# Kernel optimization log

Hardware: AMD Instinct MI355X
Metric: run time of the kernel (lower is better)

Reference implementation:

```python
import jax, jax.numpy as jnp
import numpy as np

B, H, W, DIM, WS, SHIFT, NH = 8, 64, 64, 512, 8, 4, 16
NC, NE, HID, GH = 3, 4, 2048, 256
N = WS * WS
nW = (H // WS) * (W // WS)
HD = DIM // NH
LN_EPS = 1e-5


def _static_buffers():
    # SwinV2 log-spaced continuous relative coords table
    r = np.arange(-(WS - 1), WS, dtype=np.float32)
    table = np.stack(np.meshgrid(r, r, indexing='ij'), axis=-1)[None]  # (1,2WS-1,2WS-1,2)
    table = table / (WS - 1) * 8.0
    table = np.sign(table) * np.log2(np.abs(table) + 1.0) / np.log2(8.0)
    # relative position index (N,N)
    coords = np.stack(np.meshgrid(np.arange(WS), np.arange(WS), indexing='ij'))
    cf = coords.reshape(2, -1)
    rel = (cf[:, :, None] - cf[:, None, :]).transpose(1, 2, 0).astype(np.int64)
    rel[..., 0] += WS - 1
    rel[..., 1] += WS - 1
    rel[..., 0] *= 2 * WS - 1
    rpi = rel.sum(-1)
    # shifted-window attention mask (nW,N,N)
    img = np.zeros((1, H, W, 1), np.float32)
    cnt = 0
    sls = (slice(0, -WS), slice(-WS, -SHIFT), slice(-SHIFT, None))
    for hs in sls:
        for ws_ in sls:
            img[:, hs, ws_, :] = cnt
            cnt += 1
    mw = img.reshape(1, H // WS, WS, W // WS, WS, 1).transpose(0, 1, 3, 2, 4, 5).reshape(-1, N)
    am = mw[:, None, :] - mw[:, :, None]
    am = np.where(am != 0, -100.0, 0.0).astype(np.float32)
    return jnp.asarray(table), rpi, jnp.asarray(am)

TABLE, RPI, ATTN_MASK = _static_buffers()


def _ln(x, w, b):
    m = x.mean(-1, keepdims=True)
    v = ((x - m) ** 2).mean(-1, keepdims=True)
    return (x - m) / jnp.sqrt(v + LN_EPS) * w + b


def setup_inputs():
    key = jax.random.key(0)
    ks = iter(jax.random.split(key, 40))
    p = lambda shape: jax.random.normal(next(ks), shape, jnp.float32) * 0.02
    return {
        'x': jax.random.normal(next(ks), (B, H * W, DIM), jnp.float32),
        'qkv_w': p((3 * DIM, DIM)), 'q_bias': p((DIM,)), 'v_bias': p((DIM,)),
        'logit_scale': jnp.log(10.0 * jnp.ones((NH, 1, 1), jnp.float32)),
        'cpb_w1': p((512, 2)), 'cpb_b1': p((512,)), 'cpb_w2': p((NH, 512)),
        'proj_w': p((DIM, DIM)), 'proj_b': jnp.zeros((DIM,), jnp.float32),
        'norm1_w': jnp.ones((DIM,), jnp.float32), 'norm1_b': jnp.zeros((DIM,), jnp.float32),
        'norm2_w': jnp.ones((DIM,), jnp.float32), 'norm2_b': jnp.zeros((DIM,), jnp.float32),
        'exp_w1': p((NE, HID, DIM)), 'exp_b1': jnp.zeros((NE, HID), jnp.float32),
        'exp_w2': p((NE, DIM, HID)), 'exp_b2': jnp.zeros((NE, DIM), jnp.float32),
        'gate_l1_w': p((GH, DIM)), 'gate_l1_b': jnp.zeros((GH,), jnp.float32),
        'gate_fa_w': p((GH, GH)), 'gate_fa_b': jnp.zeros((GH,), jnp.float32),
        'gate_l2_w': p((NE, GH)), 'gate_l2_b': jnp.zeros((NE,), jnp.float32),
        'task_w': p((DIM, DIM)), 'task_b': jnp.zeros((DIM,), jnp.float32),
    }


def reference(x, qkv_w, q_bias, v_bias, logit_scale, cpb_w1, cpb_b1, cpb_w2,
              proj_w, proj_b, norm1_w, norm1_b, norm2_w, norm2_b,
              exp_w1, exp_b1, exp_w2, exp_b2,
              gate_l1_w, gate_l1_b, gate_fa_w, gate_fa_b, gate_l2_w, gate_l2_b,
              task_w, task_b):
    shortcut = x
    # cyclic shift + window partition
    xi = jnp.roll(x.reshape(B, H, W, DIM), (-SHIFT, -SHIFT), axis=(1, 2))
    xw = xi.reshape(B, H // WS, WS, W // WS, WS, DIM).transpose(0, 1, 3, 2, 4, 5).reshape(-1, N, DIM)
    # qkv with q/v bias only (k bias zero)
    qkv_b = jnp.concatenate([q_bias, jnp.zeros_like(v_bias), v_bias])
    qkv = (xw @ qkv_w.T + qkv_b).reshape(-1, N, 3, NH, HD).transpose(2, 0, 3, 1, 4)
    q, k, v = qkv[0], qkv[1], qkv[2]
    # SwinV2 cosine attention
    qn = q / jnp.maximum(jnp.linalg.norm(q, axis=-1, keepdims=True), 1e-12)
    kn = k / jnp.maximum(jnp.linalg.norm(k, axis=-1, keepdims=True), 1e-12)
    scale = jnp.exp(jnp.minimum(logit_scale, jnp.log(100.0)))
    attn = jnp.einsum('bhnd,bhmd->bhnm', qn, kn) * scale
    # continuous relative position bias
    bias_tbl = (jax.nn.relu(TABLE @ cpb_w1.T + cpb_b1) @ cpb_w2.T).reshape(-1, NH)
    rpb = bias_tbl[RPI.reshape(-1)].reshape(N, N, NH).transpose(2, 0, 1)
    attn = attn + (16.0 * jax.nn.sigmoid(rpb))[None]
    # shifted window mask
    attn = attn.reshape(B, nW, NH, N, N) + ATTN_MASK[None, :, None]
    attn = jax.nn.softmax(attn.reshape(-1, NH, N, N), axis=-1)
    out = jnp.einsum('bhnm,bhmd->bnhd', attn, v).reshape(-1, N, DIM)
    out = out @ proj_w.T + proj_b
    # window reverse + reverse shift
    xr = out.reshape(B, H // WS, W // WS, WS, WS, DIM).transpose(0, 1, 3, 2, 4, 5).reshape(B, H, W, DIM)
    xr = jnp.roll(xr, (SHIFT, SHIFT), axis=(1, 2)).reshape(B, H * W, DIM)
    x1 = shortcut + _ln(xr, norm1_w, norm1_b)  # SwinV2 post-norm residual
    # MMoE FFN (inference gating path; dropouts are eval no-ops)
    eo = []
    for e in range(NE):
        h = jax.nn.gelu(x1 @ exp_w1[e].T + exp_b1[e], approximate=False)
        eo.append(h @ exp_w2[e].T + exp_b2[e])
    eo = jnp.stack(eo, axis=-1)  # (B, L, DIM, NE)
    t = x1 @ task_w.T + task_b
    g = jax.nn.relu(t @ gate_l1_w.T + gate_l1_b)
    aw = jax.nn.softmax(g @ gate_fa_w.T + gate_fa_b, axis=-1)
    gate_logits = (g * aw) @ gate_l2_w.T + gate_l2_b
    wts = jax.nn.softmax(gate_logits, axis=-1)  # temperature = 1.0
    moe = jnp.einsum('blde,ble->bld', eo, wts)
    return x1 + _ln(moe, norm2_w, norm2_b)
```

## Files before the change

### kernel.cpp

```cpp
#include <hip/hip_runtime.h>
#include <math.h>

typedef __bf16 bf16;
typedef bf16 bf16x8 __attribute__((ext_vector_type(8)));
typedef bf16 bf16x4_t __attribute__((ext_vector_type(4)));
typedef float f32x4 __attribute__((ext_vector_type(4)));


#define EPI_QKV  0
#define EPI_PROJ 1
#define EPI_BF16 2
#define EPI_RELU 3
#define EPI_F32  4
#define EPI_GELU 5
#define EPI_MOE  6

#define NIN 26

#define GLDS16(gp, lp)                                                    \
    __builtin_amdgcn_global_load_lds(                                     \
        (const __attribute__((address_space(1))) void*)(gp),              \
        (__attribute__((address_space(3))) void*)(lp), 16, 0, 0)

__global__ __launch_bounds__(256) void probe_k(const unsigned short* __restrict__ x,
                                               int* __restrict__ flag)
{
    __shared__ int cnt[256];
    int t = threadIdx.x;
    int bad = 0;
    for (int j = t; j < 4096; j += 256) {
        int e = (x[j] >> 7) & 0xFF;
        if (e >= 132) bad++;
    }
    cnt[t] = bad;
    __syncthreads();
    for (int s = 128; s > 0; s >>= 1) {
        if (t < s) cnt[t] += cnt[t + s];
        __syncthreads();
    }
    if (t == 0) *flag = (cnt[0] > 64) ? 1 : 0;
}

struct ConvArgs {
    const void* src[NIN];
    bf16* dst[NIN];
    int n[NIN];
};

__global__ __launch_bounds__(256) void conv_k(ConvArgs a, const int* __restrict__ flag)
{
    int i = blockIdx.y;
    int n4 = a.n[i] >> 2;
    bf16x4_t* dst = (bf16x4_t*)a.dst[i];
    int stride = gridDim.x * 256;
    if (*flag) {
        const float4* s = (const float4*)a.src[i];
        for (int j = blockIdx.x * 256 + threadIdx.x; j < n4; j += stride) {
            float4 v = s[j];
            dst[j] = (bf16x4_t){(bf16)v.x, (bf16)v.y, (bf16)v.z, (bf16)v.w};
        }
    } else {
        const bf16x4_t* s = (const bf16x4_t*)a.src[i];
        for (int j = blockIdx.x * 256 + threadIdx.x; j < n4; j += stride)
            dst[j] = s[j];
    }
}

__device__ __forceinline__ int win_remap(int r) {
    int win = r >> 6, tok = r & 63;
    int b = win >> 6, wi = win & 63;
    int h = (((wi >> 3) << 3) + (tok >> 3) + 4) & 63;
    int w = (((wi & 7) << 3) + (tok & 7) + 4) & 63;
    return (b << 12) | (h << 6) | w;
}

template<int REMAP_A, int EPI>
__global__ __launch_bounds__(256, 4) void gemm_k(
    const bf16* __restrict__ A, const bf16* __restrict__ Bw,
    void* __restrict__ Cout,
    const bf16* __restrict__ bias, const bf16* __restrict__ bias2,
    const float* __restrict__ wts, int N, int K, int eIdx, int nbm)
{
    __shared__ __attribute__((aligned(16))) bf16 As[128 * 64];
    __shared__ __attribute__((aligned(16))) bf16 Bs[128 * 64];
    const int tid = threadIdx.x;

    const int lin = blockIdx.x;
    const int nbn = N >> 7;
    const int xcd = lin & 7, s = lin >> 3;
    const int nbmx = nbm >> 3;
    const int G = nbmx < 16 ? nbmx : 16;
    const int gsz = G * nbn;
    const int gi = s / gsz, rem = s - gi * gsz;
    const int bn = rem / G, bmi = rem - bn * G;
    const int bm = xcd + 8 * (gi * G + bmi);

    const int wave = tid >> 6, lane = tid & 63;
    const int wm = (wave >> 1) << 6, wn = (wave & 1) << 6;
    const int lrow = lane & 15, quad = lane >> 4;

    const int sr = tid >> 3, sc = tid & 7;
    const int scg = sc ^ (sr & 7);
    int ga[4];
#pragma unroll
    for (int i = 0; i < 4; i++) {
        int r = bm * 128 + sr + i * 32;
        ga[i] = REMAP_A ? win_remap(r) : r;
    }
    const int brow = bn * 128 + sr;
    bf16* lA = As + tid * 8;
    bf16* lB = Bs + tid * 8;

    f32x4 acc[4][4];
#pragma unroll
    for (int i = 0; i < 4; i++)
#pragma unroll
        for (int j = 0; j < 4; j++) acc[i][j] = (f32x4){0.f, 0.f, 0.f, 0.f};

    for (int k0 = 0; k0 < K; k0 += 64) {
        __syncthreads();
#pragma unroll
        for (int i = 0; i < 4; i++) {
            GLDS16(A + (size_t)ga[i] * K + k0 + scg * 8, lA + i * 2048);
            GLDS16(Bw + (size_t)(brow + i * 32) * K + k0 + scg * 8, lB + i * 2048);
        }
        __syncthreads();
#pragma unroll
        for (int ks = 0; ks < 2; ks++) {
            bf16x8 af[4], bfr[4];
#pragma unroll
            for (int t = 0; t < 4; t++) {
                int ra = wm + t * 16 + lrow;
                af[t] = *(const bf16x8*)(&As[ra * 64 + (((ks << 2) + quad) ^ (ra & 7)) * 8]);
                int rb = wn + t * 16 + lrow;
                bfr[t] = *(const bf16x8*)(&Bs[rb * 64 + (((ks << 2) + quad) ^ (rb & 7)) * 8]);
            }
#pragma unroll
            for (int tm = 0; tm < 4; tm++)
#pragma unroll
                for (int tn = 0; tn < 4; tn++)
                    acc[tm][tn] = __builtin_amdgcn_mfma_f32_16x16x32_bf16(
                        af[tm], bfr[tn], acc[tm][tn], 0, 0, 0);
        }
    }

    const int cr0 = quad << 2, cc0 = lane & 15;
#pragma unroll
    for (int tm = 0; tm < 4; tm++) {
#pragma unroll
        for (int r = 0; r < 4; r++) {
            int row = bm * 128 + wm + tm * 16 + cr0 + r;
            float wr;
            if constexpr (EPI == EPI_GELU) wr = wts[(size_t)row * 4 + eIdx];
#pragma unroll
            for (int tn = 0; tn < 4; tn++) {
                int col = bn * 128 + wn + tn * 16 + cc0;
                float v = acc[tm][tn][r];
                if constexpr (EPI == EPI_QKV) {
                    float bv = 0.f;
                    if (col < 512) bv = (float)bias[col];
                    else if (col >= 1024) bv = (float)bias2[col - 1024];
                    ((bf16*)Cout)[(size_t)row * N + col] = (bf16)(v + bv);
                } else if constexpr (EPI == EPI_PROJ) {
                    v += (float)bias[col];
                    ((bf16*)Cout)[(size_t)win_remap(row) * N + col] = (bf16)v;
                } else if constexpr (EPI == EPI_BF16) {
                    v += (float)bias[col];
                    ((bf16*)Cout)[(size_t)row * N + col] = (bf16)v;
                } else if constexpr (EPI == EPI_RELU) {
                    v += (float)bias[col];
                    ((bf16*)Cout)[(size_t)row * N + col] = (bf16)fmaxf(v, 0.f);
                } else if constexpr (EPI == EPI_F32) {
                    v += (float)bias[col];
                    ((float*)Cout)[(size_t)row * N + col] = v;
                } else if constexpr (EPI == EPI_GELU) {
                    v += (float)bias[col];
                    float u = 1.5957691216f * v * fmaf(0.044715f * v, v, 1.0f);
                    float g = v * __builtin_amdgcn_rcpf(1.0f + __expf(-u));
                    g *= wr;
                    ((bf16*)Cout)[(size_t)row * N + col] = (bf16)g;
                } else if constexpr (EPI == EPI_MOE) {
                    float* p = &((float*)Cout)[(size_t)row * N + col];
                    if (eIdx == 0) *p = v; else *p += v;
                }
            }
        }
    }
}

__global__ __launch_bounds__(64) void cpb_k(const bf16* __restrict__ w1,
                                            const bf16* __restrict__ b1,
                                            const bf16* __restrict__ w2,
                                            float* __restrict__ tbl)
{
    int e = blockIdx.x;
    int d0 = e / 15, d1 = e % 15;
    auto f = [](int d) -> float {
        float v = (float)(d - 7) * (8.0f / 7.0f);
        float t = log2f(fabsf(v) + 1.0f) * (1.0f / 3.0f);
        return v < 0.f ? -t : (v > 0.f ? t : 0.0f);
    };
    float t0 = f(d0), t1 = f(d1);
    __shared__ float hsh[512];
    int tid = threadIdx.x;
    for (int j = tid; j < 512; j += 64) {
        float h = t0 * (float)w1[j * 2 + 0] + t1 * (float)w1[j * 2 + 1] + (float)b1[j];
        hsh[j] = fmaxf(h, 0.0f);
    }
    __syncthreads();
    if (tid < 16) {
        float sum = 0.f;
        for (int j = 0; j < 512; j++) sum += hsh[j] * (float)w2[tid * 512 + j];
        tbl[e * 16 + tid] = 16.0f / (1.0f + expf(-sum));
    }
}

__global__ __launch_bounds__(256) void expand_k(const float* __restrict__ tbl,
                                                float* __restrict__ mbt)
{
    int head = blockIdx.x & 15, cls = blockIdx.x >> 4;
    int eh = cls >> 1, ew = cls & 1;
    for (int idx = threadIdx.x; idx < 4096; idx += 256) {
        int m = idx >> 6, n = idx & 63;
        int qi = m >> 3, qj = m & 7, ki = n >> 3, kj = n & 7;
        float bias = tbl[((qi - ki + 7) * 15 + (qj - kj + 7)) * 16 + head];
        int qid = (eh ? (qi < 4 ? 1 : 2) : 0) * 3 + (ew ? (qj < 4 ? 1 : 2) : 0);
        int kid = (eh ? (ki < 4 ? 1 : 2) : 0) * 3 + (ew ? (kj < 4 ? 1 : 2) : 0);
        mbt[(size_t)blockIdx.x * 4096 + idx] = bias + (qid != kid ? -100.f : 0.f);
    }
}

#define PT 72
#define VT 72
__global__ __launch_bounds__(64) void attn_k(const bf16* __restrict__ qkv,
                                             const bf16* __restrict__ lsc,
                                             const float* __restrict__ mbt,
                                             bf16* __restrict__ aout)
{
    __shared__ __attribute__((aligned(16))) bf16 Vt[32 * VT];
    __shared__ __attribute__((aligned(16))) bf16 Ps[64 * PT];
    const int lane = threadIdx.x;
    const int pair = blockIdx.x;
    const int win  = pair >> 4, head = pair & 15;

    const int lcol = lane & 15;
    const int quad = lane >> 4;
    const int lk   = quad << 3;

    const bf16* qbase = qkv + (size_t)(win * 64) * 1536 + head * 32;

    {
        const bf16* vp = qbase + (size_t)lane * 1536 + 1024;
        bf16x8 v0 = *(const bf16x8*)(vp);
        bf16x8 v1 = *(const bf16x8*)(vp + 8);
        bf16x8 v2 = *(const bf16x8*)(vp + 16);
        bf16x8 v3 = *(const bf16x8*)(vp + 24);
#pragma unroll
        for (int j = 0; j < 8; j++) {
            Vt[(j)      * VT + lane] = v0[j];
            Vt[(j + 8)  * VT + lane] = v1[j];
            Vt[(j + 16) * VT + lane] = v2[j];
            Vt[(j + 24) * VT + lane] = v3[j];
        }
    }

    bf16x8 qf[4], kf[4];
#pragma unroll
    for (int t = 0; t < 4; t++) {
        const bf16* qp = qbase + (size_t)(t * 16 + lcol) * 1536 + lk;
        bf16x8 q = *(const bf16x8*)qp;
        float ss = 0.f;
#pragma unroll
        for (int j = 0; j < 8; j++) { float f = (float)q[j]; ss += f * f; }
        ss += __shfl_xor(ss, 16); ss += __shfl_xor(ss, 32);
        float inv = 1.f / fmaxf(sqrtf(ss), 1e-12f);
#pragma unroll
        for (int j = 0; j < 8; j++) q[j] = (bf16)((float)q[j] * inv);
        qf[t] = q;

        const bf16* kp = qbase + (size_t)(t * 16 + lcol) * 1536 + 512 + lk;
        bf16x8 k = *(const bf16x8*)kp;
        ss = 0.f;
#pragma unroll
        for (int j = 0; j < 8; j++) { float f = (float)k[j]; ss += f * f; }
        ss += __shfl_xor(ss, 16); ss += __shfl_xor(ss, 32);
        inv = 1.f / fmaxf(sqrtf(ss), 1e-12f);
#pragma unroll
        for (int j = 0; j < 8; j++) k[j] = (bf16)((float)k[j] * inv);
        kf[t] = k;
    }

    f32x4 s[4][4];
#pragma unroll
    for (int tm = 0; tm < 4; tm++)
#pragma unroll
        for (int tn = 0; tn < 4; tn++) s[tm][tn] = (f32x4){0.f, 0.f, 0.f, 0.f};
#pragma unroll
    for (int tm = 0; tm < 4; tm++)
#pragma unroll
        for (int tn = 0; tn < 4; tn++)
            s[tm][tn] = __builtin_amdgcn_mfma_f32_16x16x32_bf16(
                qf[tm], kf[tn], s[tm][tn], 0, 0, 0);

    float scale = expf(fminf((float)lsc[head], 4.6051701860f));
    int wi = win & 63, wh = wi >> 3, ww = wi & 7;
    const float* Tb = mbt +
        (((size_t)(((wh == 7) ? 2 : 0) + ((ww == 7) ? 1 : 0)) * 16 + head) << 12);
    float rinv[4][4];
#pragma unroll
    for (int tm = 0; tm < 4; tm++) {
#pragma unroll
        for (int r = 0; r < 4; r++) {
            int m = tm * 16 + quad * 4 + r;
            const float* Tm = Tb + m * 64 + lcol;
            float p0 = __expf(fmaf(s[tm][0][r], scale, Tm[0]));
            float p1 = __expf(fmaf(s[tm][1][r], scale, Tm[16]));
            float p2 = __expf(fmaf(s[tm][2][r], scale, Tm[32]));
            float p3 = __expf(fmaf(s[tm][3][r], scale, Tm[48]));
            float sum = (p0 + p1) + (p2 + p3);
            sum += __shfl_xor(sum, 1);
            sum += __shfl_xor(sum, 2);
            sum += __shfl_xor(sum, 4);
            sum += __shfl_xor(sum, 8);
            rinv[tm][r] = __builtin_amdgcn_rcpf(sum);
            Ps[m * PT + 0  + lcol] = (bf16)p0;
            Ps[m * PT + 16 + lcol] = (bf16)p1;
            Ps[m * PT + 32 + lcol] = (bf16)p2;
            Ps[m * PT + 48 + lcol] = (bf16)p3;
        }
    }
    __syncthreads();

    f32x4 o[4][2];
#pragma unroll
    for (int tm = 0; tm < 4; tm++)
#pragma unroll
        for (int tn = 0; tn < 2; tn++) o[tm][tn] = (f32x4){0.f, 0.f, 0.f, 0.f};
#pragma unroll
    for (int ks = 0; ks < 2; ks++) {
        bf16x8 af[4], vf[2];
#pragma unroll
        for (int tm = 0; tm < 4; tm++)
            af[tm] = *(const bf16x8*)(&Ps[(tm * 16 + lcol) * PT + lk + ks * 32]);
#pragma unroll
        for (int tn = 0; tn < 2; tn++)
            vf[tn] = *(const bf16x8*)(&Vt[(tn * 16 + lcol) * VT + lk + ks * 32]);
#pragma unroll
        for (int tm = 0; tm < 4; tm++)
#pragma unroll
            for (int tn = 0; tn < 2; tn++)
                o[tm][tn] = __builtin_amdgcn_mfma_f32_16x16x32_bf16(
                    af[tm], vf[tn], o[tm][tn], 0, 0, 0);
    }

    bf16* ob = aout + (size_t)(win * 64) * 512 + head * 32;
#pragma unroll
    for (int tm = 0; tm < 4; tm++)
#pragma unroll
        for (int tn = 0; tn < 2; tn++)
#pragma unroll
            for (int r = 0; r < 4; r++) {
                int m = tm * 16 + quad * 4 + r;
                ob[(size_t)m * 512 + tn * 16 + lcol] =
                    (bf16)(o[tm][tn][r] * rinv[tm][r]);
            }
}

__global__ __launch_bounds__(64) void ln_res_k(const bf16* __restrict__ xin,
                                               const bf16* __restrict__ pin,
                                               const bf16* __restrict__ w,
                                               const bf16* __restrict__ b,
                                               bf16* __restrict__ x1)
{
    int row = blockIdx.x, lane = threadIdx.x;
    bf16x8 pv = *(const bf16x8*)(pin + (size_t)row * 512 + lane * 8);
    float v[8]; float s = 0.f;
#pragma unroll
    for (int i = 0; i < 8; i++) { v[i] = (float)pv[i]; s += v[i]; }
#pragma unroll
    for (int o = 32; o >= 1; o >>= 1) s += __shfl_xor(s, o);
    float mean = s * (1.f / 512.f);
    float vv = 0.f;
#pragma unroll
    for (int i = 0; i < 8; i++) { float d = v[i] - mean; vv += d * d; }
#pragma unroll
    for (int o = 32; o >= 1; o >>= 1) vv += __shfl_xor(vv, o);
    float rstd = rsqrtf(vv * (1.f / 512.f) + 1e-5f);
    bf16x8 xv = *(const bf16x8*)(xin + (size_t)row * 512 + lane * 8);
    bf16x8 wv = *(const bf16x8*)(w + lane * 8);
    bf16x8 bv = *(const bf16x8*)(b + lane * 8);
    bf16x8 ov;
#pragma unroll
    for (int i = 0; i < 8; i++) {
        float ln = (v[i] - mean) * rstd * (float)wv[i] + (float)bv[i];
        ov[i] = (bf16)((float)xv[i] + ln);
    }
    *(bf16x8*)(x1 + (size_t)row * 512 + lane * 8) = ov;
}

__global__ __launch_bounds__(64) void final_k(const float* __restrict__ moe,
                                              const bf16* __restrict__ x1,
                                              const bf16* __restrict__ w,
                                              const bf16* __restrict__ b,
                                              const float* __restrict__ wts,
                                              const bf16* __restrict__ b2,
                                              float* __restrict__ out)
{
    int row = blockIdx.x, lane = threadIdx.x;
    float w0 = wts[row * 4 + 0], w1 = wts[row * 4 + 1],
          w2 = wts[row * 4 + 2], w3 = wts[row * 4 + 3];
    const float4* mr = (const float4*)(moe + (size_t)row * 512 + lane * 8);
    float4 m0 = mr[0], m1 = mr[1];
    float v[8] = {m0.x, m0.y, m0.z, m0.w, m1.x, m1.y, m1.z, m1.w};
    bf16x8 b20 = *(const bf16x8*)(b2 + lane * 8);
    bf16x8 b21 = *(const bf16x8*)(b2 + 512 + lane * 8);
    bf16x8 b22 = *(const bf16x8*)(b2 + 1024 + lane * 8);
    bf16x8 b23 = *(const bf16x8*)(b2 + 1536 + lane * 8);
    float s = 0.f;
#pragma unroll
    for (int i = 0; i < 8; i++) {
        v[i] += w0 * (float)b20[i] + w1 * (float)b21[i]
              + w2 * (float)b22[i] + w3 * (float)b23[i];
        s += v[i];
    }
#pragma unroll
    for (int o = 32; o >= 1; o >>= 1) s += __shfl_xor(s, o);
    float mean = s * (1.f / 512.f);
    float vv = 0.f;
#pragma unroll
    for (int i = 0; i < 8; i++) { float d = v[i] - mean; vv += d * d; }
#pragma unroll
    for (int o = 32; o >= 1; o >>= 1) vv += __shfl_xor(vv, o);
    float rstd = rsqrtf(vv * (1.f / 512.f) + 1e-5f);
    bf16x8 xv = *(const bf16x8*)(x1 + (size_t)row * 512 + lane * 8);
    bf16x8 wv = *(const bf16x8*)(w + lane * 8);
    bf16x8 bv = *(const bf16x8*)(b + lane * 8);
    float ot[8];
#pragma unroll
    for (int i = 0; i < 8; i++) {
        float ln = (v[i] - mean) * rstd * (float)wv[i] + (float)bv[i];
        ot[i] = (float)xv[i] + ln;
    }
    float4* op = (float4*)(out + (size_t)row * 512 + lane * 8);
    op[0] = (float4){ot[0], ot[1], ot[2], ot[3]};
    op[1] = (float4){ot[4], ot[5], ot[6], ot[7]};
}

__global__ __launch_bounds__(64) void gate_k(const float* __restrict__ fa,
                                             const bf16* __restrict__ g,
                                             const bf16* __restrict__ w2,
                                             const bf16* __restrict__ b2,
                                             float* __restrict__ wts)
{
    int row = blockIdx.x, lane = threadIdx.x;
    const float* fr = fa + (size_t)row * 256;
    float a[4]; float mx = -1e30f;
#pragma unroll
    for (int i = 0; i < 4; i++) { a[i] = fr[lane * 4 + i]; mx = fmaxf(mx, a[i]); }
#pragma unroll
    for (int o = 32; o >= 1; o >>= 1) mx = fmaxf(mx, __shfl_xor(mx, o));
    float sum = 0.f;
#pragma unroll
    for (int i = 0; i < 4; i++) { a[i] = expf(a[i] - mx); sum += a[i]; }
#pragma unroll
    for (int o = 32; o >= 1; o >>= 1) sum += __shfl_xor(sum, o);
    float inv = 1.f / sum;
    float gb[4];
#pragma unroll
    for (int i = 0; i < 4; i++)
        gb[i] = a[i] * inv * (float)g[(size_t)row * 256 + lane * 4 + i];
    float lg[4];
#pragma unroll
    for (int j = 0; j < 4; j++) {
        float p = 0.f;
#pragma unroll
        for (int i = 0; i < 4; i++) p += gb[i] * (float)w2[j * 256 + lane * 4 + i];
        lg[j] = p;
    }
#pragma unroll
    for (int o = 32; o >= 1; o >>= 1) {
#pragma unroll
        for (int j = 0; j < 4; j++) lg[j] += __shfl_xor(lg[j], o);
    }
    if (lane == 0) {
        float m2 = -1e30f;
#pragma unroll
        for (int j = 0; j < 4; j++) { lg[j] += (float)b2[j]; m2 = fmaxf(m2, lg[j]); }
        float s2 = 0.f; float e2[4];
#pragma unroll
        for (int j = 0; j < 4; j++) { e2[j] = expf(lg[j] - m2); s2 += e2[j]; }
#pragma unroll
        for (int j = 0; j < 4; j++) wts[(size_t)row * 4 + j] = e2[j] / s2;
    }
}

extern "C" void kernel_launch(void* const* d_in, const int* in_sizes, int n_in,
                              void* d_out, int out_size, void* d_ws, size_t ws_size,
                              hipStream_t stream)
{
    float* out = (float*)d_out;
    char* ws = (char*)d_ws;
    const size_t MB = 1024ull * 1024ull;

    static const int sizes[NIN] = {
        16777216, 786432, 512, 512, 16, 1024, 512, 8192, 262144, 512,
        512, 512, 512, 512, 4194304, 8192, 4194304, 2048,
        131072, 256, 65536, 256, 1024, 4, 262144, 512
    };
    ConvArgs ca;
    size_t off = 0;
    bf16* cp[NIN];
    for (int i = 1; i < NIN; i++) {
        cp[i] = (bf16*)(ws + off);
        off += ((size_t)sizes[i] * 2 + 255) & ~255ull;
    }
    cp[0] = (bf16*)(ws + 20 * MB);
    for (int i = 0; i < NIN; i++) {
        ca.src[i] = d_in[i];
        ca.dst[i] = cp[i];
        ca.n[i]   = sizes[i];
    }
    const bf16 *xc = cp[0], *qkv_w = cp[1], *q_bias = cp[2], *v_bias = cp[3],
               *lsc = cp[4], *cpb_w1 = cp[5], *cpb_b1 = cp[6], *cpb_w2 = cp[7],
               *proj_w = cp[8], *proj_b = cp[9], *n1w = cp[10], *n1b = cp[11],
               *n2w = cp[12], *n2b = cp[13], *exp_w1 = cp[14], *exp_b1 = cp[15],
               *exp_w2 = cp[16], *exp_b2 = cp[17], *gl1w = cp[18], *gl1b = cp[19],
               *gfaw = cp[20], *gfab = cp[21], *gl2w = cp[22], *gl2b = cp[23],
               *taskw = cp[24], *taskb = cp[25];

    bf16*  qkv   = (bf16*)(ws + 53 * MB);
    bf16*  aout  = (bf16*)(ws + 149 * MB);
    bf16*  projo = (bf16*)(ws + 53 * MB);
    bf16*  x1    = (bf16*)(ws + 20 * MB);
    bf16*  tbuf  = (bf16*)(ws + 53 * MB);
    bf16*  gbuf  = (bf16*)(ws + 85 * MB);
    float* fabuf = (float*)(ws + 101 * MB);
    float* mbt   = (float*)(ws + 52 * MB);
    int*   flag  = (int*)(ws + 181 * MB);
    float* wts   = (float*)(ws + 181 * MB + 4096);
    float* tbl   = (float*)(ws + 181 * MB + 4096 + 524288);

    const bool bigws = ws_size >= 246 * MB;
    bf16*  hid = (bf16*)(ws + 53 * MB);
    float* moe = bigws ? (float*)(ws + 182 * MB) : (float*)(ws + 117 * MB);

    probe_k<<<1, 256, 0, stream>>>((const unsigned short*)d_in[0], flag);
    conv_k<<<dim3(1024, NIN), 256, 0, stream>>>(ca, flag);

    cpb_k<<<225, 64, 0, stream>>>(cpb_w1, cpb_b1, cpb_w2, tbl);
    expand_k<<<64, 256, 0, stream>>>(tbl, mbt);
    gemm_k<1, EPI_QKV><<<256 * 12, 256, 0, stream>>>(
        xc, qkv_w, qkv, q_bias, v_bias, nullptr, 1536, 512, 0, 256);
    attn_k<<<8192, 64, 0, stream>>>(qkv, lsc, mbt, aout);
    gemm_k<0, EPI_PROJ><<<256 * 4, 256, 0, stream>>>(
        aout, proj_w, projo, proj_b, nullptr, nullptr, 512, 512, 0, 256);
    ln_res_k<<<32768, 64, 0, stream>>>(xc, projo, n1w, n1b, x1);
    gemm_k<0, EPI_BF16><<<256 * 4, 256, 0, stream>>>(
        x1, taskw, tbuf, taskb, nullptr, nullptr, 512, 512, 0, 256);
    gemm_k<0, EPI_RELU><<<256 * 2, 256, 0, stream>>>(
        tbuf, gl1w, gbuf, gl1b, nullptr, nullptr, 256, 512, 0, 256);
    gemm_k<0, EPI_F32><<<256 * 2, 256, 0, stream>>>(
        gbuf, gfaw, fabuf, gfab, nullptr, nullptr, 256, 256, 0, 256);
    gate_k<<<32768, 64, 0, stream>>>(fabuf, gbuf, gl2w, gl2b, wts);

    if (bigws) {
        for (int e = 0; e < 4; e++) {
            gemm_k<0, EPI_GELU><<<256 * 16, 256, 0, stream>>>(
                x1, exp_w1 + (size_t)e * 2048 * 512, hid,
                exp_b1 + e * 2048, nullptr, wts, 2048, 512, e, 256);
            gemm_k<0, EPI_MOE><<<256 * 4, 256, 0, stream>>>(
                hid, exp_w2 + (size_t)e * 512 * 2048, moe,
                nullptr, nullptr, nullptr, 512, 2048, e, 256);
        }
    } else {
        for (int e = 0; e < 4; e++) {
            for (int h = 0; h < 2; h++) {
                const size_t ro = (size_t)h * 16384;
                gemm_k<0, EPI_GELU><<<128 * 16, 256, 0, stream>>>(
                    x1 + ro * 512, exp_w1 + (size_t)e * 2048 * 512, hid,
                    exp_b1 + e * 2048, nullptr, wts + ro * 4, 2048, 512, e, 128);
                gemm_k<0, EPI_MOE><<<128 * 4, 256, 0, stream>>>(
                    hid, exp_w2 + (size_t)e * 512 * 2048, moe + ro * 512,
                    nullptr, nullptr, nullptr, 512, 2048, e, 128);
            }
        }
    }
    final_k<<<32768, 64, 0, stream>>>(moe, x1, n2w, n2b, wts, exp_b2, out);
}
```

Measured before the change: 1.138 ms.

## Add 256x256-tile double-buffered GEMM kernel for MoE expert FFN

Adds a new GEMM kernel with 256x256 output tiles, 512 threads (8 waves each computing 128x64), and double-buffered LDS staged through direct global-to-LDS loads with an XOR swizzle. It uses an XCD-aware grouped block mapping. The expert up- and down-projections now use this kernel in place of the 128-tile gemm_k. The larger tiles raise arithmetic intensity and cut redundant global reads for the dominant FFN GEMMs. The costs are high register pressure from 32 accumulators per lane and large LDS use (128KB per block), which limits occupancy. The down-projection launches only 256 or 128 blocks, which may underfill the GPU.

After: 1.307 ms. +14.9%, slower.

```diff
diff --git a/kernel.cpp b/kernel.cpp
--- a/kernel.cpp
+++ b/kernel.cpp
@@ -21,6 +21,8 @@
     __builtin_amdgcn_global_load_lds(                                     \
         (const __attribute__((address_space(1))) void*)(gp),              \
         (__attribute__((address_space(3))) void*)(lp), 16, 0, 0)
+
+#define MEMFENCE asm volatile("" ::: "memory")
 
 __global__ __launch_bounds__(256) void probe_k(const unsigned short* __restrict__ x,
                                                int* __restrict__ flag)
@@ -188,6 +190,124 @@
     }
 }
 
+template<int EPI>
+__global__ __launch_bounds__(512, 2) void gemm256_k(
+    const bf16* __restrict__ A, const bf16* __restrict__ Bw,
+    void* __restrict__ Cout,
+    const bf16* __restrict__ bias, const float* __restrict__ wts,
+    int N, int K, int eIdx, int nbm)
+{
+    __shared__ __attribute__((aligned(16))) bf16 LDS[2][2][256 * 64];
+    const int tid = threadIdx.x;
+
+    const int lin = blockIdx.x;
+    const int nbn = N >> 8;
+    const int xcd = lin & 7, s = lin >> 3;
+    const int nbmx = nbm >> 3;
+    const int G = nbmx < 16 ? nbmx : 16;
+    const int gsz = G * nbn;
+    const int gi = s / gsz, rem = s - gi * gsz;
+    const int bn = rem / G, bmi = rem - bn * G;
+    const int bm = xcd + 8 * (gi * G + bmi);
+
+    const int wave = tid >> 6, lane = tid & 63;
+    const int wr_ = wave >> 2, wc_ = wave & 3;
+    const int wm = wr_ * 128, wn = wc_ * 64;
+    const int lrow = lane & 15, quad = lane >> 4;
+
+    const int sr = tid >> 3, sc = tid & 7;
+    const int scg = sc ^ (sr & 7);
+    const int arow = bm * 256 + sr;
+    const int brow = bn * 256 + sr;
+
+    f32x4 acc[8][4];
+#pragma unroll
+    for (int i = 0; i < 8; i++)
+#pragma unroll
+        for (int j = 0; j < 4; j++) acc[i][j] = (f32x4){0.f, 0.f, 0.f, 0.f};
+
+    auto stage = [&](int buf, int k0) {
+#pragma unroll
+        for (int i = 0; i < 4; i++) {
+            GLDS16(A + (size_t)(arow + i * 64) * K + k0 + scg * 8,
+                   &LDS[buf][0][tid * 8 + i * 4096]);
+            GLDS16(Bw + (size_t)(brow + i * 64) * K + k0 + scg * 8,
+                   &LDS[buf][1][tid * 8 + i * 4096]);
+        }
+    };
+
+    const int nk = K >> 6;
+    stage(0, 0);
+    stage(1, 64);
+    asm volatile("s_waitcnt vmcnt(8)" ::: "memory");
+    __builtin_amdgcn_s_barrier();
+    MEMFENCE;
+
+    int cur = 0;
+    for (int t = 0; t < nk; ++t) {
+        const bf16* As = &LDS[cur][0][0];
+        const bf16* Bs = &LDS[cur][1][0];
+#pragma unroll
+        for (int ks = 0; ks < 2; ks++) {
+            bf16x8 af[8], bfr[4];
+#pragma unroll
+            for (int tm = 0; tm < 8; tm++) {
+                int ra = wm + tm * 16 + lrow;
+                af[tm] = *(const bf16x8*)(&As[ra * 64 + (((ks << 2) + quad) ^ (ra & 7)) * 8]);
+            }
+#pragma unroll
+            for (int tn = 0; tn < 4; tn++) {
+                int rb = wn + tn * 16 + lrow;
+                bfr[tn] = *(const bf16x8*)(&Bs[rb * 64 + (((ks << 2) + quad) ^ (rb & 7)) * 8]);
+            }
+#pragma unroll
+            for (int tm = 0; tm < 8; tm++)
+#pragma unroll
+                for (int tn = 0; tn < 4; tn++)
+                    acc[tm][tn] = __builtin_amdgcn_mfma_f32_16x16x32_bf16(
+                        af[tm], bfr[tn], acc[tm][tn], 0, 0, 0);
+        }
+        MEMFENCE;
+        __builtin_amdgcn_s_barrier();
+        MEMFENCE;
+        if (t + 2 < nk) {
+            stage(cur, (t + 2) << 6);
+            asm volatile("s_waitcnt vmcnt(8)" ::: "memory");
+        } else {
+            asm volatile("s_waitcnt vmcnt(0)" ::: "memory");
+        }
+        __builtin_amdgcn_s_barrier();
+        MEMFENCE;
+        cur ^= 1;
+    }
+
+    const int cr0 = quad << 2, cc0 = lane & 15;
+#pragma unroll
+    for (int tm = 0; tm < 8; tm++) {
+#pragma unroll
+        for (int r = 0; r < 4; r++) {
+            int row = bm * 256 + wm + tm * 16 + cr0 + r;
+            float wrw;
+            if constexpr (EPI == EPI_GELU) wrw = wts[(size_t)row * 4 + eIdx];
+#pragma unroll
+            for (int tn = 0; tn < 4; tn++) {
+                int col = bn * 256 + wn + tn * 16 + cc0;
+                float v = acc[tm][tn][r];
+                if constexpr (EPI == EPI_GELU) {
+                    v += (float)bias[col];
+                    float u = 1.5957691216f * v * fmaf(0.044715f * v, v, 1.0f);
+                    float g = v * __builtin_amdgcn_rcpf(1.0f + __expf(-u));
+                    g *= wrw;
+                    ((bf16*)Cout)[(size_t)row * N + col] = (bf16)g;
+                } else {
+                    float* p = &((float*)Cout)[(size_t)row * N + col];
+                    if (eIdx == 0) *p = v; else *p += v;
+                }
+            }
+        }
+    }
+}
+
 __global__ __launch_bounds__(64) void cpb_k(const bf16* __restrict__ w1,
                                             const bf16* __restrict__ b1,
                                             const bf16* __restrict__ w2,
@@ -565,23 +685,23 @@
 
     if (bigws) {
         for (int e = 0; e < 4; e++) {
-            gemm_k<0, EPI_GELU><<<256 * 16, 256, 0, stream>>>(
+            gemm256_k<EPI_GELU><<<1024, 512, 0, stream>>>(
                 x1, exp_w1 + (size_t)e * 2048 * 512, hid,
-                exp_b1 + e * 2048, nullptr, wts, 2048, 512, e, 256);
-            gemm_k<0, EPI_MOE><<<256 * 4, 256, 0, stream>>>(
+                exp_b1 + e * 2048, wts, 2048, 512, e, 128);
+            gemm256_k<EPI_MOE><<<256, 512, 0, stream>>>(
                 hid, exp_w2 + (size_t)e * 512 * 2048, moe,
-                nullptr, nullptr, nullptr, 512, 2048, e, 256);
+                nullptr, nullptr, 512, 2048, e, 128);
         }
     } else {
         for (int e = 0; e < 4; e++) {
             for (int h = 0; h < 2; h++) {
                 const size_t ro = (size_t)h * 16384;
-                gemm_k<0, EPI_GELU><<<128 * 16, 256, 0, stream>>>(
+                gemm256_k<EPI_GELU><<<512, 512, 0, stream>>>(
                     x1 + ro * 512, exp_w1 + (size_t)e * 2048 * 512, hid,
-                    exp_b1 + e * 2048, nullptr, wts + ro * 4, 2048, 512, e, 128);
-                gemm_k<0, EPI_MOE><<<128 * 4, 256, 0, stream>>>(
+                    exp_b1 + e * 2048, wts + ro * 4, 2048, 512, e, 64);
+                gemm256_k<EPI_MOE><<<128, 512, 0, stream>>>(
                     hid, exp_w2 + (size_t)e * 512 * 2048, moe + ro * 512,
-                    nullptr, nullptr, nullptr, 512, 2048, e, 128);
+                    nullptr, nullptr, 512, 2048, e, 64);
             }
         }
     }
```
